# Kernel tuning notes

Measured on AMD Instinct MI355X. Metric: run time of the kernel, lower is better.

Reference implementation:

```python
import jax, jax.numpy as jnp
import numpy as np

B, T, F, H, OUT, SEQ, LA = 512, 80, 32, 512, 2, 64, 16
RS, RE = 4, 6  # replace_start, replace_end


def _lstm_cell(x, h, c, w_ih, w_hh, b_ih, b_hh):
    # PyTorch LSTMCell: gates ordered (i, f, g, o)
    g = x @ w_ih.T + b_ih + h @ w_hh.T + b_hh  # [B, 4H]
    i, f, gg, o = jnp.split(g, 4, axis=1)
    i, f, o = jax.nn.sigmoid(i), jax.nn.sigmoid(f), jax.nn.sigmoid(o)
    c2 = f * c + i * jnp.tanh(gg)
    h2 = o * jnp.tanh(c2)
    return h2, c2


def setup_inputs() -> dict:
    key = jax.random.key(0)
    ks = jax.random.split(key, 16)
    s = lambda k, shape, fan: jax.random.uniform(k, shape, jnp.float32, -1.0, 1.0) / np.sqrt(fan)
    return {
        "x": jax.random.normal(ks[0], (B, T, F), jnp.float32),
        "w_ih0": s(ks[1], (4 * H, F), H), "w_hh0": s(ks[2], (4 * H, H), H),
        "b_ih0": s(ks[3], (4 * H,), H), "b_hh0": s(ks[4], (4 * H,), H),
        "w_ih1": s(ks[5], (4 * H, H), H), "w_hh1": s(ks[6], (4 * H, H), H),
        "b_ih1": s(ks[7], (4 * H,), H), "b_hh1": s(ks[8], (4 * H,), H),
        "fc1_w": s(ks[9], (H, H), H), "fc1_b": s(ks[10], (H,), H),
        "fc2_w": s(ks[11], (H, H), H), "fc2_b": s(ks[12], (H,), H),
        "fc3_w": s(ks[13], (OUT, H), H), "fc3_b": s(ks[14], (OUT,), H),
    }


def reference(x, w_ih0, w_hh0, b_ih0, b_hh0, w_ih1, w_hh1, b_ih1, b_hh1,
              fc1_w, fc1_b, fc2_w, fc2_b, fc3_w, fc3_b):
    def stack(x_t, state):
        h0, c0, h1, c1 = state
        h0, c0 = _lstm_cell(x_t, h0, c0, w_ih0, w_hh0, b_ih0, b_hh0)
        h1, c1 = _lstm_cell(h0, h1, c1, w_ih1, w_hh1, b_ih1, b_hh1)
        return (h0, c0, h1, c1)

    def head(h):
        y = jax.nn.gelu(h @ fc1_w.T + fc1_b, approximate=False)
        y = jax.nn.gelu(y @ fc2_w.T + fc2_b, approximate=False)
        return y @ fc3_w.T + fc3_b  # [B, OUT]

    z = jnp.zeros((B, H), x.dtype)
    state0 = (z, z, z, z)

    # Warmup over the first SEQ steps (strictly sequential -> lax.scan).
    xs_warm = jnp.swapaxes(x[:, :SEQ, :], 0, 1)  # [SEQ, B, F]
    state = jax.lax.scan(lambda s, xt: (stack(xt, s), None), state0, xs_warm)[0]
    out0 = head(state[2])  # h of last layer

    xs_fc = jnp.swapaxes(x[:, SEQ:, :], 0, 1)  # [LA, B, F]

    def step(carry, x_t):
        state, out = carry
        x_t = x_t.at[:, RS:RE].set(out)
        state = stack(x_t, state)
        out = head(state[2])
        return (state, out), out

    _, outs = jax.lax.scan(step, (state, out0), xs_fc)  # [LA, B, OUT]
    outputs = jnp.concatenate([out0[None], outs], axis=0)  # [LA+1, B, OUT]
    return jnp.swapaxes(outputs, 0, 1)  # [B, LA+1, OUT]
```

## Files before the change

### kernel.cpp

```cpp
#include <hip/hip_runtime.h>
#include <math.h>

typedef short s16x4 __attribute__((ext_vector_type(4)));
typedef short s16x8 __attribute__((ext_vector_type(8)));
typedef float f32x4 __attribute__((ext_vector_type(4)));
typedef unsigned short us;
typedef unsigned long long ull;

#define WAITVM(N) do { asm volatile("s_waitcnt vmcnt(" #N ")" ::: "memory"); __builtin_amdgcn_sched_barrier(0); } while (0)

namespace {
constexpr int T = 80, Fdim = 32, H = 512, OSTR = 34;
constexpr int CH = 2048;

__device__ __forceinline__ us f2h(float f) {
  union { _Float16 h; us u; } x; x.h = (_Float16)f; return x.u;
}
__device__ __forceinline__ float sigf(float v) { return 1.f / (1.f + expf(-v)); }
__device__ __forceinline__ float geluf(float v) {
  return 0.5f * v * (1.f + erff(v * 0.70710678118654752f));
}

__device__ __forceinline__ ull ald8(const void* p) {
  return __hip_atomic_load((const ull*)p, __ATOMIC_RELAXED, __HIP_MEMORY_SCOPE_AGENT);
}
__device__ __forceinline__ void ast8(void* p, ull v) {
  __hip_atomic_store((ull*)p, v, __ATOMIC_RELAXED, __HIP_MEMORY_SCOPE_AGENT);
}
__device__ __forceinline__ void ast4f(float* p, float v) {
  __hip_atomic_store(p, v, __ATOMIC_RELAXED, __HIP_MEMORY_SCOPE_AGENT);
}

union U8 { ull u; s16x4 v4; float f[2]; };
union S8 { s16x8 v; ull u[2]; };

struct SetA { ull a0, a1; };
struct SetB { s16x8 b1, b0; };
struct HSetA { ull a0; };
struct HSetB { s16x8 b0, b1; };

__global__ __launch_bounds__(256)
void pack_w_kernel(const float* __restrict__ w1, const float* __restrict__ w2,
                   int K1, int K2, int NKC, int head, us* __restrict__ dst) {
  int bid = blockIdx.x;
  int jb = bid / NKC, kc = bid % NKC;
  int tid = threadIdx.x;
  int strip = tid >> 6, l = tid & 63;
  int nl = l & 15, kg = l >> 4;
  int n = head ? (jb * 64 + strip * 16 + nl) : (strip * 512 + jb * 16 + nl);
  s16x8 h8;
  #pragma unroll
  for (int i = 0; i < 8; ++i) {
    int k = kc * 32 + kg * 8 + i;
    float v = (k < K1) ? w1[(size_t)n * K1 + k] : w2[(size_t)n * K2 + (k - K1)];
    h8[i] = (short)f2h(v);
  }
  *(s16x8*)&dst[(size_t)bid * CH + strip * 512 + l * 8] = h8;
}

__global__ __launch_bounds__(256)
void bsum_kernel(const float* bi0, const float* bh0, const float* bi1, const float* bh1,
                 float* bs0, float* bs1) {
  int i = blockIdx.x * 256 + threadIdx.x;
  if (i < 2048) bs0[i] = bi0[i] + bh0[i];
  else { int j = i - 2048; bs1[j] = bi1[j] + bh1[j]; }
}

__global__ __launch_bounds__(256, 1)
void persist_kernel(const float* __restrict__ x,
                    const us* __restrict__ Wp0, const us* __restrict__ Wp1,
                    const us* __restrict__ Wpf1, const us* __restrict__ Wpf2,
                    const float* __restrict__ bs0, const float* __restrict__ bs1,
                    const float* __restrict__ fc1_b, const float* __restrict__ fc2_b,
                    const float* __restrict__ fc3_w, const float* __restrict__ fc3_b,
                    us* hp0_0, us* hp0_1, us* hp1_0, us* hp1_1,
                    float* c0, float* c1, us* y1p,
                    float* out, int* cnt)
{
  __shared__ __align__(16) us Ash[8][2048];
  __shared__ __align__(16) float Gs[4][64][16];

  const int tid = threadIdx.x;
  const int bid = blockIdx.x;
  const int w = tid >> 6, l = tid & 63;
  const int m = bid >> 5;
  const int lb = bid & 31;
  const int jb = (lb & 7) * 4 + (lb >> 3);
  const int row0 = m * 64;
  const int j0 = jb * 16;
  const int base31 = j0 & 31;

  const us* WpJ0 = Wp0 + (size_t)jb * 17 * CH;
  const us* WpJ1 = Wp1 + (size_t)jb * 32 * CH;

  int ph = 0;
  auto garrive = [&]() {
    ++ph;
    WAITVM(0);
    __syncthreads();
    if (tid == 0)
      __hip_atomic_store(&cnt[m * 512 + lb * 16], ph, __ATOMIC_RELEASE,
                         __HIP_MEMORY_SCOPE_AGENT);
  };
  auto gwait = [&]() {
    if (tid < 32) {
      while (__hip_atomic_load(&cnt[m * 512 + tid * 16], __ATOMIC_RELAXED,
                               __HIP_MEMORY_SCOPE_AGENT) < ph)
        __builtin_amdgcn_s_sleep(1);
      __builtin_amdgcn_fence(__ATOMIC_ACQUIRE, "workgroup");
    }
    __syncthreads();
  };

  auto fused = [&](bool DO1, bool DO0, int t, bool use_fb, int kidx, bool preh) {
    const us* h0prev = ((t + 1) & 1) ? hp0_1 : hp0_0;
    const us* h1prev = (t & 1) ? hp1_1 : hp1_0;
    us* h1w = ((t + 1) & 1) ? hp1_1 : hp1_0;
    us* h0w = (t & 1) ? hp0_1 : hp0_0;

    f32x4 acc0[4], acc1[4];
    #pragma unroll
    for (int mf = 0; mf < 4; ++mf) {
      acc0[mf] = {0.f, 0.f, 0.f, 0.f};
      acc1[mf] = {0.f, 0.f, 0.f, 0.f};
    }
    const int NP = DO1 ? 32 : 16;
    SetA A0s, A1s, A2s, A3s;
    SetB B0s, B1s, B2s, B3s;

    auto issA = [&](int c, SetA& R, int hi) {
      if (c >= hi) return;
      const us* a = ((c < 16) ? h0prev : h1prev) + (size_t)(m * 16 + (c & 15)) * CH;
      R.a0 = ald8(a + tid * 8);
      R.a1 = ald8(a + tid * 8 + 4);
    };
    auto issB = [&](int c, SetB& R, int hi) {
      if (c >= hi) return;
      if (DO1) R.b1 = *(const s16x8*)(WpJ1 + (size_t)c * CH + w * 512 + l * 8);
      if (DO0 && c < 16)
        R.b0 = *(const s16x8*)(WpJ0 + (size_t)(c + 1) * CH + w * 512 + l * 8);
    };
    auto wrtA = [&](int c, SetA& R, int hi) {
      if (c >= hi) return;
      int sl = c & 7;
      *(ull*)&Ash[sl][tid * 8] = R.a0;
      *(ull*)&Ash[sl][tid * 8 + 4] = R.a1;
    };
    auto lcomp = [&](int kc, SetB& B, bool c1on, bool c0on) {
      int sl = kc & 7;
      #pragma unroll
      for (int mf = 0; mf < 4; ++mf) {
        s16x8 Ah = *(const s16x8*)&Ash[sl][mf * 512 + l * 8];
        if (c1on)
          acc1[mf] = __builtin_amdgcn_mfma_f32_16x16x32_f16(Ah, B.b1, acc1[mf], 0, 0, 0);
        if (c0on)
          acc0[mf] = __builtin_amdgcn_mfma_f32_16x16x32_f16(Ah, B.b0, acc0[mf], 0, 0, 0);
      }
    };

    auto runseg = [&](int lo, int hi) {
      issA(lo + 0, A0s, hi); issA(lo + 1, A1s, hi);
      issA(lo + 2, A2s, hi); issA(lo + 3, A3s, hi);
      wrtA(lo + 0, A0s, hi); wrtA(lo + 1, A1s, hi);
      wrtA(lo + 2, A2s, hi); wrtA(lo + 3, A3s, hi);
      issA(lo + 4, A0s, hi); issA(lo + 5, A1s, hi);
      issA(lo + 6, A2s, hi); issA(lo + 7, A3s, hi);
      __syncthreads();
      for (int base = lo; base < hi; base += 4) {
        { int kc = base + 0; lcomp(kc, B0s, DO1, DO0 && kc < 16); issB(kc + 4, B0s, hi); }
        { int kc = base + 1; lcomp(kc, B1s, DO1, DO0 && kc < 16); issB(kc + 4, B1s, hi); }
        { int kc = base + 2; lcomp(kc, B2s, DO1, DO0 && kc < 16); issB(kc + 4, B2s, hi); }
        { int kc = base + 3; lcomp(kc, B3s, DO1, DO0 && kc < 16); issB(kc + 4, B3s, hi); }
        __syncthreads();
        wrtA(base + 4, A0s, hi); wrtA(base + 5, A1s, hi);
        wrtA(base + 6, A2s, hi); wrtA(base + 7, A3s, hi);
        issA(base + 8, A0s, hi); issA(base + 9, A1s, hi);
        issA(base + 10, A2s, hi); issA(base + 11, A3s, hi);
        __syncthreads();
      }
    };

    if (preh) {
      if (DO1) {
        issB(16, B0s, 32); issB(17, B1s, 32); issB(18, B2s, 32); issB(19, B3s, 32);
        runseg(16, 32);
        issB(0, B0s, 16); issB(1, B1s, 16); issB(2, B2s, 16); issB(3, B3s, 16);
        gwait();
        runseg(0, 16);
      } else {
        issB(0, B0s, 16); issB(1, B1s, 16); issB(2, B2s, 16); issB(3, B3s, 16);
        runseg(0, 16);
        gwait();
      }
    } else {
      issB(0, B0s, NP); issB(1, B1s, NP); issB(2, B2s, NP); issB(3, B3s, NP);
      gwait();
      runseg(0, NP);
    }

    if (DO0) {
      SetB Bx;
      Bx.b0 = *(const s16x8*)(WpJ0 + w * 512 + l * 8);
      int srow = tid >> 2, skg = tid & 3;
      const float* xp = x + (size_t)(row0 + srow) * (T * Fdim) + (size_t)t * Fdim + skg * 8;
      float v[8];
      #pragma unroll
      for (int i = 0; i < 8; ++i) v[i] = xp[i];
      if (use_fb && skg == 0) {
        const float* op = out + (size_t)(row0 + srow) * OSTR + kidx * 2;
        v[4] = __hip_atomic_load(op, __ATOMIC_RELAXED, __HIP_MEMORY_SCOPE_AGENT);
        v[5] = __hip_atomic_load(op + 1, __ATOMIC_RELAXED, __HIP_MEMORY_SCOPE_AGENT);
      }
      s16x8 h8;
      #pragma unroll
      for (int i = 0; i < 8; ++i) h8[i] = (short)f2h(v[i]);
      int slane = skg * 16 + (srow & 15), smf = srow >> 4;
      *(s16x8*)&Ash[0][smf * 512 + slane * 8] = h8;
      __syncthreads();
      lcomp(0, Bx, false, true);
    }

    auto epi = [&](f32x4* acc, const float* bsum, float* cst, us* hw) {
      __syncthreads();
      float bsv = bsum[w * 512 + j0 + (l & 15)];
      #pragma unroll
      for (int mf = 0; mf < 4; ++mf)
        #pragma unroll
        for (int r = 0; r < 4; ++r)
          Gs[w][mf * 16 + (l >> 4) * 4 + r][l & 15] = acc[mf][r] + bsv;
      __syncthreads();
      int r = tid >> 2, sub = tid & 3, cc0 = sub * 4;
      float gvi[4], gvf[4], gvg[4], gvo[4], cv[4], cn[4], hv[4];
      #pragma unroll
      for (int q = 0; q < 4; ++q) {
        gvi[q] = Gs[0][r][cc0 + q]; gvf[q] = Gs[1][r][cc0 + q];
        gvg[q] = Gs[2][r][cc0 + q]; gvo[q] = Gs[3][r][cc0 + q];
      }
      size_t cix = (size_t)(row0 + r) * H + j0 + cc0;
      float4 cold = *(const float4*)&cst[cix];
      cv[0] = cold.x; cv[1] = cold.y; cv[2] = cold.z; cv[3] = cold.w;
      #pragma unroll
      for (int q = 0; q < 4; ++q) {
        float c2 = sigf(gvf[q]) * cv[q] + sigf(gvi[q]) * tanhf(gvg[q]);
        cn[q] = c2;
        hv[q] = sigf(gvo[q]) * tanhf(c2);
      }
      *(float4*)&cst[cix] = make_float4(cn[0], cn[1], cn[2], cn[3]);
      int kk = base31 + cc0;
      int kg = kk >> 3, i0 = kk & 7;
      int mf = r >> 4;
      int lane2 = kg * 16 + (r & 15);
      us* bb = hw + (size_t)(m * 16 + (j0 >> 5)) * CH;
      U8 hh;
      #pragma unroll
      for (int q = 0; q < 4; ++q) hh.v4[q] = (short)f2h(hv[q]);
      ast8(bb + (size_t)mf * 512 + lane2 * 8 + i0, hh.u);
      __syncthreads();
    };
    if (DO1) epi(acc1, bs1, c1, h1w);
    if (DO0) epi(acc0, bs0, c0, h0w);
  };

  auto headg = [&](const us* apack, const us* Wp, const float* bias,
                   us* yp, int kidx) {
    if (lb < 16) {
      const int mhl = lb >> 3, cb = lb & 7;
      const int hrow0 = row0 + mhl * 32, hj0 = cb * 64;
      const int wm = w >> 1, wn = w & 1;
      f32x4 hacc[2];
      hacc[0] = {0.f, 0.f, 0.f, 0.f};
      hacc[1] = {0.f, 0.f, 0.f, 0.f};
      HSetA HA0, HA1, HA2, HA3;
      HSetB HB0, HB1;
      auto hissA = [&](int c, HSetA& R) {
        if (c >= 16) return;
        const us* a = apack + (size_t)(m * 16 + c) * CH + mhl * 1024;
        R.a0 = ald8(a + tid * 4);
      };
      auto hissB = [&](int c, HSetB& R) {
        if (c >= 16) return;
        const us* b = Wp + (size_t)(cb * 16 + c) * CH + wn * 1024 + l * 8;
        R.b0 = *(const s16x8*)(b);
        R.b1 = *(const s16x8*)(b + 512);
      };
      auto hwrtA = [&](int c, HSetA& R) {
        if (c >= 16) return;
        int sl = c % 3;
        *(ull*)&Ash[sl][tid * 4] = R.a0;
      };
      auto hcmp = [&](int sl, HSetB& B) {
        s16x8 Ah = *(const s16x8*)&Ash[sl][wm * 512 + l * 8];
        hacc[0] = __builtin_amdgcn_mfma_f32_16x16x32_f16(Ah, B.b0, hacc[0], 0, 0, 0);
        hacc[1] = __builtin_amdgcn_mfma_f32_16x16x32_f16(Ah, B.b1, hacc[1], 0, 0, 0);
      };
      hissA(0, HA0); hissA(1, HA1); hissA(2, HA2); hissA(3, HA3);
      hwrtA(0, HA0); hissA(4, HA0);
      hwrtA(1, HA1); hissA(5, HA1);
      hissB(0, HB0); hissB(1, HB1);
      __syncthreads();
      for (int base = 0; base < 16; base += 4) {
        { int kc = base + 0; hcmp(kc % 3, HB0); hissB(kc + 2, HB0);
          hwrtA(kc + 2, HA2); hissA(kc + 6, HA2); __syncthreads(); }
        { int kc = base + 1; hcmp(kc % 3, HB1); hissB(kc + 2, HB1);
          hwrtA(kc + 2, HA3); hissA(kc + 6, HA3); __syncthreads(); }
        { int kc = base + 2; hcmp(kc % 3, HB0); hissB(kc + 2, HB0);
          hwrtA(kc + 2, HA0); hissA(kc + 6, HA0); __syncthreads(); }
        { int kc = base + 3; hcmp(kc % 3, HB1); hissB(kc + 2, HB1);
          hwrtA(kc + 2, HA1); hissA(kc + 6, HA1); __syncthreads(); }
      }
      __syncthreads();
      float* GsF = (float*)Gs;
      #pragma unroll
      for (int nf = 0; nf < 2; ++nf)
        #pragma unroll
        for (int rq = 0; rq < 4; ++rq) {
          int rr = wm * 16 + (l >> 4) * 4 + rq;
          int ccl = wn * 32 + nf * 16 + (l & 15);
          GsF[rr * 64 + ccl] = geluf(hacc[nf][rq] + bias[hj0 + ccl]);
        }
      __syncthreads();
      if (yp) {
        int chunk = tid >> 7, tt = tid & 127;
        int mf_loc = tt >> 6, lane = tt & 63;
        int row = mf_loc * 16 + (lane & 15);
        int kg = lane >> 4;
        S8 hv;
        #pragma unroll
        for (int i = 0; i < 8; ++i)
          hv.v[i] = (short)f2h(GsF[row * 64 + chunk * 32 + kg * 8 + i]);
        us* dst = yp + ((size_t)m * 16 + (cb * 2 + chunk)) * CH;
        ast8(dst + (size_t)(mhl * 2 + mf_loc) * 512 + lane * 8, hv.u[0]);
        ast8(dst + (size_t)(mhl * 2 + mf_loc) * 512 + lane * 8 + 4, hv.u[1]);
      } else {
        int r = tid >> 3, cg = tid & 7;
        float p0 = 0.f, p1 = 0.f;
        #pragma unroll
        for (int i = 0; i < 8; ++i) {
          float yv = GsF[r * 64 + cg * 8 + i];
          int col = hj0 + cg * 8 + i;
          p0 += yv * fc3_w[col];
          p1 += yv * fc3_w[512 + col];
        }
        #pragma unroll
        for (int d = 4; d > 0; d >>= 1) {
          p0 += __shfl_down(p0, d, 8);
          p1 += __shfl_down(p1, d, 8);
        }
        if (cg == 0) {
          atomicAdd(out + (size_t)(hrow0 + r) * OSTR + kidx * 2, p0);
          atomicAdd(out + (size_t)(hrow0 + r) * OSTR + kidx * 2 + 1, p1);
        }
      }
      __syncthreads();
    }
  };

  auto h1buf = [&](int t) { return (t & 1) ? hp1_1 : hp1_0; };

  fused(false, true, 0, false, 0, true); garrive();
  for (int t = 1; t < 64; ++t) { fused(true, true, t, false, 0, false); garrive(); }
  fused(true, false, 64, false, 0, false); garrive();

  for (int kidx = 0; kidx < 17; ++kidx) {
    const us* h1cur = h1buf(63 + kidx);
    gwait();
    headg(h1cur, Wpf1, fc1_b, y1p, kidx);
    if (lb == 16 && tid < 128) {
      int r2 = tid >> 1, o = tid & 1;
      ast4f(out + (size_t)(row0 + r2) * OSTR + kidx * 2 + o, fc3_b[o]);
    }
    garrive();
    gwait();
    headg(y1p, Wpf2, fc2_b, nullptr, kidx);
    garrive();
    if (kidx < 16) {
      fused(false, true, 64 + kidx, true, kidx, true); garrive();
      fused(true, false, 65 + kidx, false, 0, true); garrive();
    }
  }
}

}

extern "C" void kernel_launch(void* const* d_in, const int* in_sizes, int n_in,
                              void* d_out, int out_size, void* d_ws, size_t ws_size,
                              hipStream_t stream) {
  const float* x     = (const float*)d_in[0];
  const float* w_ih0 = (const float*)d_in[1];
  const float* w_hh0 = (const float*)d_in[2];
  const float* b_ih0 = (const float*)d_in[3];
  const float* b_hh0 = (const float*)d_in[4];
  const float* w_ih1 = (const float*)d_in[5];
  const float* w_hh1 = (const float*)d_in[6];
  const float* b_ih1 = (const float*)d_in[7];
  const float* b_hh1 = (const float*)d_in[8];
  const float* fc1_w = (const float*)d_in[9];
  const float* fc1_b = (const float*)d_in[10];
  const float* fc2_w = (const float*)d_in[11];
  const float* fc2_b = (const float*)d_in[12];
  const float* fc3_w = (const float*)d_in[13];
  const float* fc3_b = (const float*)d_in[14];
  float* out = (float*)d_out;
  char* wsb = (char*)d_ws;

  constexpr size_t KB = 1024;
  constexpr size_t O_WP0  = 0;
  constexpr size_t O_WP1  = 2228224;
  constexpr size_t O_WPF1 = O_WP1 + 4194304;
  constexpr size_t O_WPF2 = O_WPF1 + 524288;
  constexpr size_t O_BS0  = O_WPF2 + 524288;
  constexpr size_t O_BS1  = O_BS0 + 8192;
  constexpr size_t O_CNT  = O_BS1 + 8192;
  constexpr size_t O_HP0B = O_CNT + 16384;
  constexpr size_t O_HP1B = O_HP0B + 512 * KB;
  constexpr size_t O_C0   = O_HP1B + 512 * KB;
  constexpr size_t O_C1   = O_C0 + 1024 * KB;
  constexpr size_t O_HP0A = O_C1 + 1024 * KB;
  constexpr size_t O_HP1A = O_HP0A + 512 * KB;
  constexpr size_t O_Y1P  = O_HP1A + 512 * KB;

  us* Wp0  = (us*)(wsb + O_WP0);
  us* Wp1  = (us*)(wsb + O_WP1);
  us* Wpf1 = (us*)(wsb + O_WPF1);
  us* Wpf2 = (us*)(wsb + O_WPF2);
  float* bs0 = (float*)(wsb + O_BS0);
  float* bs1 = (float*)(wsb + O_BS1);
  int* cnt   = (int*)(wsb + O_CNT);
  us* hp0_1 = (us*)(wsb + O_HP0B);
  us* hp1_1 = (us*)(wsb + O_HP1B);
  float* c0 = (float*)(wsb + O_C0);
  float* c1 = (float*)(wsb + O_C1);
  us* hp0_0 = (us*)(wsb + O_HP0A);
  us* hp1_0 = (us*)(wsb + O_HP1A);
  us* y1p   = (us*)(wsb + O_Y1P);

  pack_w_kernel<<<dim3(32 * 17), 256, 0, stream>>>(w_ih0, w_hh0, 32, 512, 17, 0, Wp0);
  pack_w_kernel<<<dim3(32 * 32), 256, 0, stream>>>(w_ih1, w_hh1, 512, 512, 32, 0, Wp1);
  pack_w_kernel<<<dim3(8 * 16), 256, 0, stream>>>(fc1_w, fc1_w, 512, 512, 16, 1, Wpf1);
  pack_w_kernel<<<dim3(8 * 16), 256, 0, stream>>>(fc2_w, fc2_w, 512, 512, 16, 1, Wpf2);
  bsum_kernel<<<dim3(16), 256, 0, stream>>>(b_ih0, b_hh0, b_ih1, b_hh1, bs0, bs1);
  hipMemsetAsync(wsb + O_CNT, 0, 16384 + 3 * 1024 * KB, stream);

  persist_kernel<<<dim3(256), dim3(256), 0, stream>>>(
      x, Wp0, Wp1, Wpf1, Wpf2, bs0, bs1, fc1_b, fc2_b, fc3_w, fc3_b,
      hp0_0, hp0_1, hp1_0, hp1_1, c0, c1, y1p, out, cnt);
}
```

Before: 1.522 ms.

## Replace global barrier waits with per-chunk dependency polling in LSTM steps

Swaps the full all-block wait before each recurrent GEMM for fine-grained polling of only the producer blocks whose h-chunks are about to be loaded. Each K-chunk is waited on just before its prefetch, so compute on ready chunks can overlap with slower producers. A full barrier is still kept before the epilogue, and the wait targets are offset per phase for the look-ahead steps. The intent is to cut stall time at the barrier, at the cost of more polling traffic and a subtle correctness dependence on the phase offsets.

```diff
diff --git a/kernel.cpp b/kernel.cpp
--- a/kernel.cpp
+++ b/kernel.cpp
@@ -102,17 +102,32 @@
       __hip_atomic_store(&cnt[m * 512 + lb * 16], ph, __ATOMIC_RELEASE,
                          __HIP_MEMORY_SCOPE_AGENT);
   };
-  auto gwait = [&]() {
+  auto gwaitall = [&](int need) {
     if (tid < 32) {
       while (__hip_atomic_load(&cnt[m * 512 + tid * 16], __ATOMIC_RELAXED,
-                               __HIP_MEMORY_SCOPE_AGENT) < ph)
+                               __HIP_MEMORY_SCOPE_AGENT) < need)
         __builtin_amdgcn_s_sleep(1);
       __builtin_amdgcn_fence(__ATOMIC_ACQUIRE, "workgroup");
     }
     __syncthreads();
   };
-
-  auto fused = [&](bool DO1, bool DO0, int t, bool use_fb, int kidx, bool preh) {
+  auto pollH = [&](int c0, int cN, int hi, int need) {
+    if (tid < 2 * cN) {
+      int c = c0 + (tid >> 1);
+      if (c < hi) {
+        int cc = c & 15;
+        int jbw = 2 * cc + (tid & 1);
+        int lbw = ((jbw & 3) << 3) + (jbw >> 2);
+        while (__hip_atomic_load(&cnt[m * 512 + lbw * 16], __ATOMIC_RELAXED,
+                                 __HIP_MEMORY_SCOPE_AGENT) < need)
+          __builtin_amdgcn_s_sleep(1);
+        __builtin_amdgcn_fence(__ATOMIC_ACQUIRE, "workgroup");
+      }
+    }
+  };
+
+  auto fused = [&](bool DO1, bool DO0, int t, bool use_fb, int kidx,
+                   int d0, int d1, bool seg1first) {
     const us* h0prev = ((t + 1) & 1) ? hp0_1 : hp0_0;
     const us* h1prev = (t & 1) ? hp1_1 : hp1_0;
     us* h1w = ((t + 1) & 1) ? hp1_1 : hp1_0;
@@ -125,6 +140,7 @@
       acc1[mf] = {0.f, 0.f, 0.f, 0.f};
     }
     const int NP = DO1 ? 32 : 16;
+    const int need0 = ph + d0, need1 = ph + d1;
     SetA A0s, A1s, A2s, A3s;
     SetB B0s, B1s, B2s, B3s;
 
@@ -158,7 +174,9 @@
       }
     };
 
-    auto runseg = [&](int lo, int hi) {
+    auto runseg = [&](int lo, int hi, int need) {
+      pollH(lo, 8, hi, need);
+      __syncthreads();
       issA(lo + 0, A0s, hi); issA(lo + 1, A1s, hi);
       issA(lo + 2, A2s, hi); issA(lo + 3, A3s, hi);
       wrtA(lo + 0, A0s, hi); wrtA(lo + 1, A1s, hi);
@@ -171,6 +189,7 @@
         { int kc = base + 1; lcomp(kc, B1s, DO1, DO0 && kc < 16); issB(kc + 4, B1s, hi); }
         { int kc = base + 2; lcomp(kc, B2s, DO1, DO0 && kc < 16); issB(kc + 4, B2s, hi); }
         { int kc = base + 3; lcomp(kc, B3s, DO1, DO0 && kc < 16); issB(kc + 4, B3s, hi); }
+        pollH(base + 8, 4, hi, need);
         __syncthreads();
         wrtA(base + 4, A0s, hi); wrtA(base + 5, A1s, hi);
         wrtA(base + 6, A2s, hi); wrtA(base + 7, A3s, hi);
@@ -180,25 +199,22 @@
       }
     };
 
-    if (preh) {
-      if (DO1) {
-        issB(16, B0s, 32); issB(17, B1s, 32); issB(18, B2s, 32); issB(19, B3s, 32);
-        runseg(16, 32);
-        issB(0, B0s, 16); issB(1, B1s, 16); issB(2, B2s, 16); issB(3, B3s, 16);
-        gwait();
-        runseg(0, 16);
-      } else {
-        issB(0, B0s, 16); issB(1, B1s, 16); issB(2, B2s, 16); issB(3, B3s, 16);
-        runseg(0, 16);
-        gwait();
-      }
+    if (DO1 && seg1first) {
+      issB(16, B0s, 32); issB(17, B1s, 32); issB(18, B2s, 32); issB(19, B3s, 32);
+      runseg(16, 32, need1);
+      issB(0, B0s, 16); issB(1, B1s, 16); issB(2, B2s, 16); issB(3, B3s, 16);
+      runseg(0, 16, need0);
+    } else if (DO1) {
+      issB(0, B0s, 32); issB(1, B1s, 32); issB(2, B2s, 32); issB(3, B3s, 32);
+      runseg(0, 32, need0);
     } else {
-      issB(0, B0s, NP); issB(1, B1s, NP); issB(2, B2s, NP); issB(3, B3s, NP);
-      gwait();
-      runseg(0, NP);
-    }
-
+      issB(0, B0s, 16); issB(1, B1s, 16); issB(2, B2s, 16); issB(3, B3s, 16);
+      runseg(0, 16, need0);
+    }
+
+    bool waited = false;
     if (DO0) {
+      if (use_fb) { gwaitall(ph); waited = true; }
       SetB Bx;
       Bx.b0 = *(const s16x8*)(WpJ0 + w * 512 + l * 8);
       int srow = tid >> 2, skg = tid & 3;
@@ -219,6 +235,8 @@
       __syncthreads();
       lcomp(0, Bx, false, true);
     }
+
+    if (!waited) gwaitall(ph);
 
     auto epi = [&](f32x4* acc, const float* bsum, float* cst, us* hw) {
       __syncthreads();
@@ -357,25 +375,25 @@
 
   auto h1buf = [&](int t) { return (t & 1) ? hp1_1 : hp1_0; };
 
-  fused(false, true, 0, false, 0, true); garrive();
-  for (int t = 1; t < 64; ++t) { fused(true, true, t, false, 0, false); garrive(); }
-  fused(true, false, 64, false, 0, false); garrive();
+  fused(false, true, 0, false, 0, 0, 0, false); garrive();
+  for (int t = 1; t < 64; ++t) { fused(true, true, t, false, 0, 0, 0, false); garrive(); }
+  fused(true, false, 64, false, 0, 0, -1, true); garrive();
 
   for (int kidx = 0; kidx < 17; ++kidx) {
     const us* h1cur = h1buf(63 + kidx);
-    gwait();
+    gwaitall(ph);
     headg(h1cur, Wpf1, fc1_b, y1p, kidx);
     if (lb == 16 && tid < 128) {
       int r2 = tid >> 1, o = tid & 1;
       ast4f(out + (size_t)(row0 + r2) * OSTR + kidx * 2 + o, fc3_b[o]);
     }
     garrive();
-    gwait();
+    gwaitall(ph);
     headg(y1p, Wpf2, fc2_b, nullptr, kidx);
     garrive();
     if (kidx < 16) {
-      fused(false, true, 64 + kidx, true, kidx, true); garrive();
-      fused(true, false, 65 + kidx, false, 0, true); garrive();
+      fused(false, true, 64 + kidx, true, kidx, -3, 0, false); garrive();
+      fused(true, false, 65 + kidx, false, 0, 0, -3, true); garrive();
     }
   }
 }
```

Result: slower. 1.882 ms (+23.6%).
